# Performance work log

Hardware: AMD Instinct MI355X
Metric: run time of the kernel (lower is better)

## Reference

```python
import jax, jax.numpy as jnp
import numpy as np

W_BIJ, W_ORTH, W_LAP, W_PRE = 1000.0, 1000.0, 1.0, 100000.0
N, V, C, K = 8, 5000, 128, 128
NUM_DESC = int(C * 0.2)  # 25, matches sub_pre=0.2


def setup_inputs() -> dict:
    key = jax.random.key(0)
    ks = jax.random.split(key, 10)
    return {
        "C12": jax.random.normal(ks[0], (N, K, K), jnp.float32) * 0.1,
        "C21": jax.random.normal(ks[1], (N, K, K), jnp.float32) * 0.1,
        "feat_1": jax.random.normal(ks[2], (N, V, C), jnp.float32),
        "feat_2": jax.random.normal(ks[3], (N, V, C), jnp.float32),
        "evecs_1": jax.random.normal(ks[4], (N, V, K), jnp.float32) * 0.02,
        "evecs_2": jax.random.normal(ks[5], (N, V, K), jnp.float32) * 0.02,
        "evecs_trans1": jax.random.normal(ks[6], (N, K, V), jnp.float32) * 0.02,
        "evecs_trans2": jax.random.normal(ks[7], (N, K, V), jnp.float32) * 0.02,
        "evals_1": jax.random.uniform(ks[8], (N, K), jnp.float32),
        "evals_2": jax.random.uniform(ks[9], (N, K), jnp.float32),
        "desc_ind": jnp.arange(NUM_DESC, dtype=jnp.int32),
    }


def _frob3(a, b):
    # torch FrobeniusLoss on [N,K,K]: mean over batch of sum((a-b)^2, dims (1,2))
    return jnp.mean(jnp.sum((a - b) ** 2, axis=(1, 2)))


def reference(C12, C21, feat_1, feat_2, evecs_1, evecs_2,
              evecs_trans1, evecs_trans2, evals_1, evals_2, desc_ind):
    n, k, _ = C12.shape
    eye = jnp.eye(k, dtype=C12.dtype)[None]  # broadcasts over batch

    l_bij = (_frob3(jnp.einsum('nij,njk->nik', C12, C21), eye)
             + _frob3(jnp.einsum('nij,njk->nik', C21, C12), eye)) * W_BIJ

    l_orth = (_frob3(jnp.einsum('nji,njk->nik', C12, C12), eye)
              + _frob3(jnp.einsum('nji,njk->nik', C21, C21), eye)) * W_ORTH

    # diag-scale commutativity: C * evals (col scale) vs evals * C (row scale)
    l_lap = (_frob3(C12 * evals_1[:, None, :], evals_2[:, :, None] * C12)
             + _frob3(C21 * evals_2[:, None, :], evals_1[:, :, None] * C21)) * W_LAP

    # descriptor preservation via commutativity, D = num_desc subsampled channels
    f1 = feat_1[:, :, desc_ind]  # [N,V,D]
    f2 = feat_2[:, :, desc_ind]
    # M[n,d] = Phi_trans @ diag(f[:,d]) @ Phi  (KxK per descriptor), fused einsum
    M1 = jnp.einsum('nkv,nvd,nvj->ndkj', evecs_trans1, f1, evecs_1)
    M2 = jnp.einsum('nkv,nvd,nvj->ndkj', evecs_trans2, f2, evecs_2)
    s1 = jnp.einsum('nij,ndjk->ndik', C12, M1)  # C12 @ M1_d
    t1 = jnp.einsum('ndij,njk->ndik', M2, C12)  # M2_d @ C12
    s2 = jnp.einsum('nij,ndjk->ndik', C21, M2)
    t2 = jnp.einsum('ndij,njk->ndik', M1, C21)
    # torch FrobeniusLoss on 5D [N,D,1,K,K]: sum over axes (1,2), then global mean
    # over remaining [N,K,K] -> total_sum / (N*K*K)
    denom = jnp.asarray(n * k * k, s1.dtype)
    l_pre = ((jnp.sum((s1 - t1) ** 2) + jnp.sum((s2 - t2) ** 2)) / denom) * W_PRE

    return jnp.stack([l_bij, l_orth, l_lap, l_pre])
```

## Files before the change

### kernel.cpp

```cpp
#include <hip/hip_runtime.h>

typedef float v4f __attribute__((ext_vector_type(4)));
typedef unsigned int u32;
typedef __attribute__((ext_vector_type(2))) u32 u32x2;
typedef __attribute__((ext_vector_type(4))) u32 u32x4;
typedef __attribute__((ext_vector_type(8))) short bhalf8;

#define K 128
#define W_BIJ 1000.0f
#define W_ORTH 1000.0f
#define W_LAP 1.0f
#define W_PRE 100000.0f

#define NCH 79
#define TILE_B 16384
#define CTILE_B 32768
#define VPAD 5120

union B8 { u32x4 u; bhalf8 h; };

static __device__ __forceinline__ unsigned short f2b(float x) {
    union { float f; unsigned int u; } v; v.f = x;
    unsigned int u = v.u + 0x7FFFu + ((v.u >> 16) & 1u);
    return (unsigned short)(u >> 16);
}
static __device__ __forceinline__ u32 pk2(float lo, float hi) {
    return (u32)f2b(lo) | ((u32)f2b(hi) << 16);
}
static __device__ __forceinline__ float bitsf(u32 x) {
    union { u32 u; float f; } v; v.u = x; return v.f;
}
static __device__ __forceinline__ u32 cvtpk(float lo, float hi) {
    u32 r; asm("v_cvt_pk_bf16_f32 %0, %1, %2" : "=v"(r) : "v"(lo), "v"(hi)); return r;
}
static __device__ __forceinline__ void gload_lds16(const void* g, void* l) {
    __builtin_amdgcn_global_load_lds((const __attribute__((address_space(1))) u32*)g,
                                     (__attribute__((address_space(3))) u32*)l, 16, 0, 0);
}

extern "C" __global__ __launch_bounds__(256, 2)
void surfm_conv(const float* __restrict__ T1, const float* __restrict__ T2,
                const float* __restrict__ E1, const float* __restrict__ E2,
                const float* __restrict__ F1, const float* __restrict__ F2,
                const float* __restrict__ C12g, const float* __restrict__ C21g,
                const int* __restrict__ desc,
                unsigned short* __restrict__ Abf, unsigned short* __restrict__ Ebf,
                float* __restrict__ Fbf, char* __restrict__ Cbf,
                int V, int CF)
{
    __shared__ char csm[36992];
    const int b = blockIdx.x;
    const int tid = threadIdx.x;

    if (b < 1264) {
        const int c  = b % NCH;
        const int mn = b / NCH;
        const float* src = ((mn & 8) ? T2 : T1) + (size_t)(mn & 7) * K * V;
        char* dst = (char*)Abf + (size_t)b * TILE_B;
        #pragma unroll
        for (int it = 0; it < 4; ++it) {
            const int item = it * 256 + tid;
            const int grp = item & 7, r = item >> 3;
            const int kg = grp ^ (r & 7);
            const int k = c * 64 + kg * 8;
            u32x4 o = (u32x4){0u,0u,0u,0u};
            if (k + 8 <= V) {
                const v4f lo = *(const v4f*)(src + (size_t)r * V + k);
                const v4f hi = *(const v4f*)(src + (size_t)r * V + k + 4);
                o[0] = pk2(lo[0], lo[1]); o[1] = pk2(lo[2], lo[3]);
                o[2] = pk2(hi[0], hi[1]); o[3] = pk2(hi[2], hi[3]);
            }
            *(u32x4*)(dst + r * 128 + grp * 16) = o;
        }
    } else if (b < 2528) {
        const int idx = b - 1264;
        const int c  = idx % NCH;
        const int mn = idx / NCH;
        const float* src = ((mn & 8) ? E2 : E1) + (size_t)(mn & 7) * V * K;
        char* dst = (char*)Ebf + (size_t)idx * TILE_B;
        #pragma unroll
        for (int it = 0; it < 8; ++it) {
            const int item = it * 256 + tid;
            const int vp = item >> 5;
            const int j4 = (item & 31) * 4;
            const int v = c * 64 + vp * 2;
            v4f e0 = {0.f,0.f,0.f,0.f}, e1 = e0;
            if (v < V)     e0 = *(const v4f*)(src + (size_t)v * K + j4);
            if (v + 1 < V) e1 = *(const v4f*)(src + (size_t)(v + 1) * K + j4);
            #pragma unroll
            for (int e = 0; e < 4; ++e) {
                const int j = j4 + e;
                *(u32*)(csm + j * 128 + vp * 4) = pk2(e0[e], e1[e]);
            }
        }
        __syncthreads();
        #pragma unroll
        for (int it = 0; it < 4; ++it) {
            const int item = it * 256 + tid;
            *(u32x4*)(dst + item * 16) = *(const u32x4*)(csm + item * 16);
        }
    } else if (b < 2928) {
        const int idx = b - 2528;
        const int d  = idx % 25;
        const int mn = idx / 25;
        const int col = desc[d];
        const float* src = ((mn & 8) ? F2 : F1) + (size_t)(mn & 7) * V * CF + col;
        float* dst = Fbf + (size_t)idx * VPAD;
        for (int i = tid; i < VPAD; i += 256)
            dst[i] = (i < V) ? src[(size_t)i * CF] : 0.0f;
    } else {
        const int idx = b - 2928;
        const float* src = ((idx & 8) ? C21g : C12g) + (size_t)(idx & 7) * K * K;
        char* outN = Cbf + (size_t)(idx * 2 + 0) * CTILE_B;
        char* outT = Cbf + (size_t)(idx * 2 + 1) * CTILE_B;
        #pragma unroll
        for (int it = 0; it < 8; ++it) {
            const int item = it * 256 + tid;
            const int r = item >> 4, grp = item & 15;
            const int g = grp ^ (r & 7);
            const v4f lo = *(const v4f*)(src + r * K + g * 8);
            const v4f hi = *(const v4f*)(src + r * K + g * 8 + 4);
            u32x4 o;
            o[0] = pk2(lo[0], lo[1]); o[1] = pk2(lo[2], lo[3]);
            o[2] = pk2(hi[0], hi[1]); o[3] = pk2(hi[2], hi[3]);
            *(u32x4*)(outN + r * 256 + grp * 16) = o;
        }
        #pragma unroll
        for (int it = 0; it < 8; ++it) {
            const int item = it * 256 + tid;
            const int rp = item >> 5;
            const int j4 = (item & 31) * 4;
            const v4f r0 = *(const v4f*)(src + (2 * rp) * K + j4);
            const v4f r1 = *(const v4f*)(src + (2 * rp + 1) * K + j4);
            #pragma unroll
            for (int e = 0; e < 4; ++e) {
                const int j = j4 + e;
                *(u32*)(csm + j * 256 + ((rp * 4) ^ ((j & 7) << 4))) = pk2(r0[e], r1[e]);
            }
        }
        __syncthreads();
        #pragma unroll
        for (int it = 0; it < 8; ++it) {
            const int item = it * 256 + tid;
            *(u32x4*)(outT + item * 16) = *(const u32x4*)(csm + item * 16);
        }
    }
}

extern "C" __global__ __launch_bounds__(512, 4)
void surfm_stage1(const char* __restrict__ Abf, const char* __restrict__ Ebf,
                  const float* __restrict__ Fbf, char* __restrict__ MpartB)
{
    extern __shared__ char sm[];
    const int tid = threadIdx.x;
    const int l  = tid & 63;
    const int wq = __builtin_amdgcn_readfirstlane(tid >> 6);
    const int b = blockIdx.x;
    const int n = b & 7;
    const int rest = b >> 3;
    const int mat = rest & 1;
    const int vq  = (rest >> 1) & 3;
    const int dgi = rest >> 3;
    const int d0 = dgi * 2;
    const bool hasD1 = (d0 + 1) < 25;

    const int mn = mat * 8 + n;
    const char* gA = Abf + (size_t)mn * NCH * TILE_B;
    const char* gE = Ebf + (size_t)mn * NCH * TILE_B;
    const char* gW = (const char*)(Fbf + ((size_t)mn * 25 + d0) * VPAD) + vq * 5120;
    const int c0 = vq * 20;
    const int NT = (vq == 3) ? 19 : 20;

    const int lm = l & 15;
    const int lk = (l >> 4) * 8;
    const int j  = wq * 16 + lm;
    const int rkey = (lm & 7) << 4;
    float* wLds = (float*)(sm + 49152);

    v4f acc0[8], acc1[8];
    #pragma unroll
    for (int mf = 0; mf < 8; ++mf) {
        acc0[mf] = (v4f){0.f,0.f,0.f,0.f};
        acc1[mf] = (v4f){0.f,0.f,0.f,0.f};
    }

    const char* gEl = gE + j * 128 + lk * 2;

    for (int i = wq; i < 10; i += 8)
        gload_lds16(gW + (i / 5) * (VPAD * 4) + (i % 5) * 1024 + l * 16,
                    sm + 49152 + (i / 5) * 5120 + (i % 5) * 1024);
    {
        const char* tA = gA + (size_t)c0 * TILE_B;
        gload_lds16(tA + (wq * 2 + 0) * 1024 + l * 16, sm + (wq * 2 + 0) * 1024);
        gload_lds16(tA + (wq * 2 + 1) * 1024 + l * 16, sm + (wq * 2 + 1) * 1024);
    }
    u32x4 eC0 = *(const u32x4*)(gEl + (size_t)c0 * TILE_B);
    u32x4 eC1 = *(const u32x4*)(gEl + (size_t)c0 * TILE_B + 64);
    {
        const char* tA = gA + (size_t)(c0 + 1) * TILE_B;
        gload_lds16(tA + (wq * 2 + 0) * 1024 + l * 16, sm + 16384 + (wq * 2 + 0) * 1024);
        gload_lds16(tA + (wq * 2 + 1) * 1024 + l * 16, sm + 16384 + (wq * 2 + 1) * 1024);
    }
    asm volatile("s_waitcnt vmcnt(2)" ::: "memory");
    __builtin_amdgcn_s_barrier();

    #pragma unroll 1
    for (int t = 0; t < NT; ++t) {
        const int bufC = t % 3;
        u32x4 eN0 = eC0, eN1 = eC1;
        if (t + 1 < NT) {
            const char* tE = gEl + (size_t)(c0 + t + 1) * TILE_B;
            eN0 = *(const u32x4*)(tE);
            eN1 = *(const u32x4*)(tE + 64);
        }
        if (t + 2 < NT) {
            const char* tA = gA + (size_t)(c0 + t + 2) * TILE_B;
            char* dA = sm + ((t + 2) % 3) * 16384;
            gload_lds16(tA + (wq * 2 + 0) * 1024 + l * 16, dA + (wq * 2 + 0) * 1024);
            gload_lds16(tA + (wq * 2 + 1) * 1024 + l * 16, dA + (wq * 2 + 1) * 1024);
        }
        __builtin_amdgcn_sched_barrier(0);

        const char* Ab = sm + bufC * 16384;
        #pragma unroll
        for (int ks = 0; ks < 2; ++ks) {
            const u32x4 e = ks ? eC1 : eC0;
            const float* pw0 = wLds + t * 64 + ks * 32 + lk;
            const float* pw1 = pw0 + 1280;
            const v4f w0a = *(const v4f*)pw0, w0b = *(const v4f*)(pw0 + 4);
            const v4f w1a = *(const v4f*)pw1, w1b = *(const v4f*)(pw1 + 4);
            const float wl0[4] = {w0a[0], w0a[2], w0b[0], w0b[2]};
            const float wh0[4] = {w0a[1], w0a[3], w0b[1], w0b[3]};
            const float wl1[4] = {w1a[0], w1a[2], w1b[0], w1b[2]};
            const float wh1[4] = {w1a[1], w1a[3], w1b[1], w1b[3]};
            B8 p0, p1;
            #pragma unroll
            for (int t4 = 0; t4 < 4; ++t4) {
                const float elo = bitsf(e[t4] << 16);
                const float ehi = bitsf(e[t4] & 0xFFFF0000u);
                p0.u[t4] = cvtpk(elo * wl0[t4], ehi * wh0[t4]);
                if (hasD1) p1.u[t4] = cvtpk(elo * wl1[t4], ehi * wh1[t4]);
            }
            const int kb = ks * 64 + lk * 2;
            __builtin_amdgcn_s_setprio(1);
            #pragma unroll
            for (int mf = 0; mf < 8; ++mf) {
                const int r = mf * 16 + lm;
                B8 a; a.u = *(const u32x4*)(Ab + r * 128 + (kb ^ rkey));
                acc0[mf] = __builtin_amdgcn_mfma_f32_16x16x32_bf16(a.h, p0.h, acc0[mf], 0, 0, 0);
                if (hasD1)
                    acc1[mf] = __builtin_amdgcn_mfma_f32_16x16x32_bf16(a.h, p1.h, acc1[mf], 0, 0, 0);
            }
            __builtin_amdgcn_s_setprio(0);
        }
        eC0 = eN0; eC1 = eN1;

        if (t + 1 < NT) {
            if (t + 2 < NT) asm volatile("s_waitcnt vmcnt(2)" ::: "memory");
            else            asm volatile("s_waitcnt vmcnt(0)" ::: "memory");
            __builtin_amdgcn_s_barrier();
        }
    }

    const int slotM = (n * 25 + d0) * 2 + mat;
    const int rbyte = (l >> 4) * 8;
    {
        char* dst = MpartB + ((size_t)(vq * 400 + slotM)) * 32768 + j * 256 + rbyte;
        #pragma unroll
        for (int mf = 0; mf < 8; ++mf) {
            u32x2 o;
            o[0] = pk2(acc0[mf][0], acc0[mf][1]);
            o[1] = pk2(acc0[mf][2], acc0[mf][3]);
            *(u32x2*)(dst + mf * 32) = o;
        }
    }
    if (hasD1) {
        char* dst = MpartB + ((size_t)(vq * 400 + slotM + 2)) * 32768 + j * 256 + rbyte;
        #pragma unroll
        for (int mf = 0; mf < 8; ++mf) {
            u32x2 o;
            o[0] = pk2(acc1[mf][0], acc1[mf][1]);
            o[1] = pk2(acc1[mf][2], acc1[mf][3]);
            *(u32x2*)(dst + mf * 32) = o;
        }
    }
}

extern "C" __global__ __launch_bounds__(256, 2)
void surfm_mconv(const char* __restrict__ MpartB, char* __restrict__ Mbf)
{
    extern __shared__ char sm[];
    float* sMT = (float*)sm;
    const int s = blockIdx.x;
    const int tid = threadIdx.x;
    const char* p0 = MpartB + (size_t)s * 32768;
    for (int i = tid; i < 2048; i += 256) {
        const int jj = i >> 4, g = i & 15;
        float sum[8] = {0.f,0.f,0.f,0.f,0.f,0.f,0.f,0.f};
        #pragma unroll
        for (int p = 0; p < 4; ++p) {
            const u32x4 v = *(const u32x4*)(p0 + (size_t)p * 400 * 32768 + jj * 256 + g * 16);
            #pragma unroll
            for (int e = 0; e < 4; ++e) {
                sum[2 * e + 0] += bitsf(v[e] << 16);
                sum[2 * e + 1] += bitsf(v[e] & 0xFFFF0000u);
            }
        }
        float* q = sMT + jj * 132 + g * 8;
        #pragma unroll
        for (int e = 0; e < 8; ++e) q[e] = sum[e];
    }
    __syncthreads();
    char* outN = Mbf + (size_t)s * 65536;
    char* outT = outN + 32768;
    #pragma unroll
    for (int it = 0; it < 16; ++it) {
        const int item = it * 256 + tid;
        const int lay = item >> 11;
        const int g2 = item & 2047;
        const int rr = g2 >> 4, grp = g2 & 15;
        const int g = grp ^ (rr & 7);
        u32x4 o;
        if (lay == 0) {
            const float* p = sMT + rr * 132 + g * 8;
            const v4f a = *(const v4f*)p, bq = *(const v4f*)(p + 4);
            o[0] = pk2(a[0], a[1]);   o[1] = pk2(a[2], a[3]);
            o[2] = pk2(bq[0], bq[1]); o[3] = pk2(bq[2], bq[3]);
            *(u32x4*)(outT + rr * 256 + grp * 16) = o;
        } else {
            const float* p = sMT + (g * 8) * 132 + rr;
            o[0] = pk2(p[0],   p[132]); o[1] = pk2(p[264], p[396]);
            o[2] = pk2(p[528], p[660]); o[3] = pk2(p[792], p[924]);
            *(u32x4*)(outN + rr * 256 + grp * 16) = o;
        }
    }
}

extern "C" __global__ __launch_bounds__(256, 1)
void surfm_stage2(const float* __restrict__ C12g, const float* __restrict__ C21g,
                  const float* __restrict__ ev1g, const float* __restrict__ ev2g,
                  const char* __restrict__ Cbf, const char* __restrict__ Mbf,
                  float* __restrict__ out, int N, int ND)
{
    extern __shared__ char sm[];
    const int b = blockIdx.x;
    const int tid = threadIdx.x;
    const int nPre = N * ND;

    if (b < nPre) {
        const int n = b & 7, d = b >> 3;
        const size_t slot = n * 25 + d;
        const int l = tid & 63;
        const int wq = __builtin_amdgcn_readfirstlane(tid >> 6);
        const int lm = l & 15, lk = (l >> 4) * 8;
        const int wm = wq >> 1, wj = wq & 1;
        float rsum = 0.0f;

        #pragma unroll 1
        for (int ph = 0; ph < 2; ++ph) {
            const char* s0 = Cbf + ((size_t)(ph * 8 + n) * 2 + 0) * CTILE_B;
            const char* s1 = Mbf + (slot * 2 + (ph ? 1 : 0)) * 65536 + 32768;
            const char* s2 = Mbf + (slot * 2 + (ph ? 0 : 1)) * 65536;
            const char* s3 = Cbf + ((size_t)(ph * 8 + n) * 2 + 1) * CTILE_B;
            const char* gs = (wq == 0) ? s0 : (wq == 1) ? s1 : (wq == 2) ? s2 : s3;
            char* ld = sm + wq * 32768;
            if (ph) __builtin_amdgcn_s_barrier();
            #pragma unroll
            for (int i = 0; i < 32; ++i)
                gload_lds16(gs + i * 1024 + l * 16, ld + i * 1024);
            asm volatile("s_waitcnt vmcnt(0)" ::: "memory");
            __builtin_amdgcn_s_barrier();
            __builtin_amdgcn_sched_barrier(0);

            v4f as_[4][4], at_[4][4];
            #pragma unroll
            for (int mf = 0; mf < 4; ++mf)
                #pragma unroll
                for (int jf = 0; jf < 4; ++jf) {
                    as_[mf][jf] = (v4f){0.f,0.f,0.f,0.f};
                    at_[mf][jf] = (v4f){0.f,0.f,0.f,0.f};
                }
            #pragma unroll
            for (int ks = 0; ks < 4; ++ks) {
                const int kb = ks * 64 + lk * 2;
                B8 bS[4], bT[4];
                #pragma unroll
                for (int jf = 0; jf < 4; ++jf) {
                    const int jj = wj * 64 + jf * 16 + lm;
                    const int off = jj * 256 + (kb ^ ((jj & 7) << 4));
                    bS[jf].u = *(const u32x4*)(sm + 32768 + off);
                    bT[jf].u = *(const u32x4*)(sm + 98304 + off);
                }
                #pragma unroll
                for (int mf = 0; mf < 4; ++mf) {
                    const int r = wm * 64 + mf * 16 + lm;
                    const int off = r * 256 + (kb ^ ((r & 7) << 4));
                    B8 aS; aS.u = *(const u32x4*)(sm + off);
                    B8 aT; aT.u = *(const u32x4*)(sm + 65536 + off);
                    #pragma unroll
                    for (int jf = 0; jf < 4; ++jf) {
                        as_[mf][jf] = __builtin_amdgcn_mfma_f32_16x16x32_bf16(aS.h, bS[jf].h, as_[mf][jf], 0, 0, 0);
                        at_[mf][jf] = __builtin_amdgcn_mfma_f32_16x16x32_bf16(aT.h, bT[jf].h, at_[mf][jf], 0, 0, 0);
                    }
                }
            }
            #pragma unroll
            for (int mf = 0; mf < 4; ++mf)
                #pragma unroll
                for (int jf = 0; jf < 4; ++jf) {
                    const v4f df = as_[mf][jf] - at_[mf][jf];
                    rsum += df[0]*df[0] + df[1]*df[1] + df[2]*df[2] + df[3]*df[3];
                }
        }
        #pragma unroll
        for (int off = 32; off; off >>= 1) rsum += __shfl_down(rsum, off, 64);
        if (l == 0)
            atomicAdd(out + 3, rsum * (W_PRE / (float)(N * K * K)));
    } else {
        float* lds = (float*)sm;
        const int idx = b - nPre;
        const int n = idx >> 2, p = idx & 3;
        const float* c12 = C12g + (size_t)n * K * K;
        const float* c21 = C21g + (size_t)n * K * K;
        const float* Xg = (p == 1 || p == 3) ? c21 : c12;
        const float* Yg = (p == 0) ? c21 : c12;
        const float* ea = (p == 0) ? ev1g + n * K : ev2g + n * K;
        const float* eb = (p == 0) ? ev2g + n * K : ev1g + n * K;
        float* X = lds;
        float* Y = lds + K * 129;
        const int tx = tid & 15, ty = tid >> 4;
        float lap = 0.0f;
        for (int i = tid; i < K * K / 4; i += 256) {
            const int r = i >> 5, c4 = (i & 31) * 4;
            const v4f x = *(const v4f*)(Xg + r * K + c4);
            X[r * 129 + c4 + 0] = x[0]; X[r * 129 + c4 + 1] = x[1];
            X[r * 129 + c4 + 2] = x[2]; X[r * 129 + c4 + 3] = x[3];
            if (p < 2) {
                const v4f y = *(const v4f*)(Yg + r * K + c4);
                Y[r * 129 + c4 + 0] = y[0]; Y[r * 129 + c4 + 1] = y[1];
                Y[r * 129 + c4 + 2] = y[2]; Y[r * 129 + c4 + 3] = y[3];
                const float ebi = eb[r];
                #pragma unroll
                for (int e = 0; e < 4; ++e) {
                    const float dlt = ea[c4 + e] - ebi;
                    lap += x[e] * x[e] * dlt * dlt;
                }
            }
        }
        __syncthreads();
        const int i0 = ty * 8, k0 = tx * 8;
        float z[8][8];
        #pragma unroll
        for (int i = 0; i < 8; ++i)
            #pragma unroll
            for (int t = 0; t < 8; ++t) z[i][t] = 0.0f;
        for (int jj = 0; jj < K; ++jj) {
            float xi[8], yk[8];
            if (p < 2) {
                #pragma unroll
                for (int i = 0; i < 8; ++i) xi[i] = X[(i0 + i) * 129 + jj];
                #pragma unroll
                for (int t = 0; t < 8; ++t) yk[t] = Y[jj * 129 + k0 + t];
            } else {
                #pragma unroll
                for (int i = 0; i < 8; ++i) xi[i] = X[jj * 129 + i0 + i];
                #pragma unroll
                for (int t = 0; t < 8; ++t) yk[t] = X[jj * 129 + k0 + t];
            }
            #pragma unroll
            for (int i = 0; i < 8; ++i)
                #pragma unroll
                for (int t = 0; t < 8; ++t) z[i][t] += xi[i] * yk[t];
        }
        float sacc = 0.0f;
        #pragma unroll
        for (int i = 0; i < 8; ++i)
            #pragma unroll
            for (int t = 0; t < 8; ++t) {
                const float e = z[i][t] - ((i0 + i) == (k0 + t) ? 1.0f : 0.0f);
                sacc += e * e;
            }
        #pragma unroll
        for (int off = 32; off; off >>= 1) {
            sacc += __shfl_down(sacc, off, 64);
            lap  += __shfl_down(lap, off, 64);
        }
        if ((tid & 63) == 0) {
            if (p < 2) {
                atomicAdd(out + 0, sacc * (W_BIJ / (float)N));
                atomicAdd(out + 2, lap * (W_LAP / (float)N));
            } else {
                atomicAdd(out + 1, sacc * (W_ORTH / (float)N));
            }
        }
    }
}

extern "C" __global__ __launch_bounds__(256, 1)
void surfm_fused(const float* __restrict__ C12g, const float* __restrict__ C21g,
                 const float* __restrict__ F1, const float* __restrict__ F2,
                 const float* __restrict__ E1g, const float* __restrict__ E2g,
                 const float* __restrict__ T1, const float* __restrict__ T2,
                 const float* __restrict__ ev1g, const float* __restrict__ ev2g,
                 const int* __restrict__ desc, float* __restrict__ out,
                 int N, int ND, int V, int CF)
{
    extern __shared__ char smem[];
    const int b   = blockIdx.x;
    const int tid = threadIdx.x;
    const int nPre = N * ND;

    if (b < nPre) {
        const int n = b & 7;
        const int d = b >> 3;
        const int col = desc[d];
        const float* A1g = T1 + (size_t)n * K * V;
        const float* A2g = T2 + (size_t)n * K * V;
        const float* B1g = E1g + (size_t)n * V * K;
        const float* B2g = E2g + (size_t)n * V * K;
        const float* w1g = F1 + (size_t)n * V * CF;
        const float* w2g = F2 + (size_t)n * V * CF;

        char* As1 = smem;
        char* As2 = smem + 32768;
        char* Bt1 = smem + 65536;
        char* Bt2 = smem + 98304;

        const int l  = tid & 63;
        const int w  = tid >> 6;
        const int lm = l & 15;
        const int lk = (l >> 4) * 8;

        v4f acc1[8][2], acc2[8][2];
        #pragma unroll
        for (int mf = 0; mf < 8; ++mf)
            #pragma unroll
            for (int jf = 0; jf < 2; ++jf) {
                acc1[mf][jf] = (v4f){0.f,0.f,0.f,0.f};
                acc2[mf][jf] = (v4f){0.f,0.f,0.f,0.f};
            }

        for (int v0 = 0; v0 < V; v0 += 128) {
            __syncthreads();
            #pragma unroll 4
            for (int it = 0; it < 16; ++it) {
                const int i  = it * 256 + tid;
                const int r  = i >> 5;
                const int c4 = (i & 31) * 4;
                const int vg = v0 + c4;
                v4f a1 = {0.f,0.f,0.f,0.f}, a2 = {0.f,0.f,0.f,0.f};
                if (vg < V) {
                    a1 = *(const v4f*)(A1g + (size_t)r * V + vg);
                    a2 = *(const v4f*)(A2g + (size_t)r * V + vg);
                }
                const int byte = (r * 256 + c4 * 2) ^ ((r & 7) << 4);
                short4 p1, p2;
                p1.x = (short)f2b(a1[0]); p1.y = (short)f2b(a1[1]);
                p1.z = (short)f2b(a1[2]); p1.w = (short)f2b(a1[3]);
                p2.x = (short)f2b(a2[0]); p2.y = (short)f2b(a2[1]);
                p2.z = (short)f2b(a2[2]); p2.w = (short)f2b(a2[3]);
                *(short4*)(As1 + byte) = p1;
                *(short4*)(As2 + byte) = p2;
            }
            #pragma unroll 2
            for (int it = 0; it < 8; ++it) {
                const int i  = it * 256 + tid;
                const int j4 = (i & 31) * 4;
                const int vp = (i >> 5) * 2;
                const int va = v0 + vp, vb = va + 1;
                v4f e1a = {0.f,0.f,0.f,0.f}, e1b = e1a, e2a = e1a, e2b = e1a;
                if (va < V) {
                    const float w1 = w1g[(size_t)va * CF + col];
                    const float w2 = w2g[(size_t)va * CF + col];
                    e1a = *(const v4f*)(B1g + (size_t)va * K + j4) * w1;
                    e2a = *(const v4f*)(B2g + (size_t)va * K + j4) * w2;
                }
                if (vb < V) {
                    const float w1 = w1g[(size_t)vb * CF + col];
                    const float w2 = w2g[(size_t)vb * CF + col];
                    e1b = *(const v4f*)(B1g + (size_t)vb * K + j4) * w1;
                    e2b = *(const v4f*)(B2g + (size_t)vb * K + j4) * w2;
                }
                #pragma unroll
                for (int e = 0; e < 4; ++e) {
                    const int j = j4 + e;
                    const int key = (((j & 7) ^ ((j >> 3) & 7)) << 4);
                    const int byte = (j * 256 + vp * 2) ^ key;
                    *(u32*)(Bt1 + byte) = pk2(e1a[e], e1b[e]);
                    *(u32*)(Bt2 + byte) = pk2(e2a[e], e2b[e]);
                }
            }
            __syncthreads();
            #pragma unroll
            for (int ks = 0; ks < 4; ++ks) {
                const int k0 = ks * 32 + lk;
                bhalf8 bB1[2], bB2[2];
                #pragma unroll
                for (int jf = 0; jf < 2; ++jf) {
                    const int j = w * 32 + jf * 16 + lm;
                    const int key = (((j & 7) ^ ((j >> 3) & 7)) << 4);
                    const int byte = (j * 256 + k0 * 2) ^ key;
                    bB1[jf] = *(const bhalf8*)(Bt1 + byte);
                    bB2[jf] = *(const bhalf8*)(Bt2 + byte);
                }
                #pragma unroll
                for (int mf = 0; mf < 8; ++mf) {
                    const int r = mf * 16 + lm;
                    const int byte = (r * 256 + k0 * 2) ^ ((r & 7) << 4);
                    const bhalf8 a1 = *(const bhalf8*)(As1 + byte);
                    const bhalf8 a2 = *(const bhalf8*)(As2 + byte);
                    acc1[mf][0] = __builtin_amdgcn_mfma_f32_16x16x32_bf16(a1, bB1[0], acc1[mf][0], 0, 0, 0);
                    acc1[mf][1] = __builtin_amdgcn_mfma_f32_16x16x32_bf16(a1, bB1[1], acc1[mf][1], 0, 0, 0);
                    acc2[mf][0] = __builtin_amdgcn_mfma_f32_16x16x32_bf16(a2, bB2[0], acc2[mf][0], 0, 0, 0);
                    acc2[mf][1] = __builtin_amdgcn_mfma_f32_16x16x32_bf16(a2, bB2[1], acc2[mf][1], 0, 0, 0);
                }
            }
        }
        __syncthreads();
        float* M1 = (float*)smem;
        float* M2 = (float*)smem + K * K;
        #pragma unroll
        for (int mf = 0; mf < 8; ++mf)
            #pragma unroll
            for (int jf = 0; jf < 2; ++jf)
                #pragma unroll
                for (int rg = 0; rg < 4; ++rg) {
                    const int row = mf * 16 + ((l >> 4) << 2) + rg;
                    const int cj  = w * 32 + jf * 16 + lm;
                    const int pc  = ((((cj >> 2) ^ ((row >> 3) & 7)) << 2) | (cj & 3));
                    M1[row * K + pc] = acc1[mf][jf][rg];
                    M2[row * K + pc] = acc2[mf][jf][rg];
                }
        __syncthreads();

        const int tx = tid & 15, ty = tid >> 4;
        const int r0 = ty * 8;
        const int ca = tx * 4, cb = 64 + tx * 4;
        const int kcol = ty & 7;
        const float* c12 = C12g + (size_t)n * K * K;
        const float* c21 = C21g + (size_t)n * K * K;
        v4f acc1a[8], acc1b[8], acc2a[8], acc2b[8];
        #pragma unroll
        for (int i = 0; i < 8; ++i) {
            acc1a[i] = (v4f){0,0,0,0}; acc1b[i] = (v4f){0,0,0,0};
            acc2a[i] = (v4f){0,0,0,0}; acc2b[i] = (v4f){0,0,0,0};
        }
        for (int jj = 0; jj < K; ++jj) {
            const int keyj = (jj >> 3) & 7;
            const int ga = (tx ^ keyj) << 2;
            const int gb = ((16 + tx) ^ keyj) << 2;
            const v4f m1ra = *(const v4f*)(M1 + jj * K + ga);
            const v4f m1rb = *(const v4f*)(M1 + jj * K + gb);
            const v4f m2ra = *(const v4f*)(M2 + jj * K + ga);
            const v4f m2rb = *(const v4f*)(M2 + jj * K + gb);
            const v4f c12ra = *(const v4f*)(c12 + jj * K + ca);
            const v4f c12rb = *(const v4f*)(c12 + jj * K + cb);
            const v4f c21ra = *(const v4f*)(c21 + jj * K + ca);
            const v4f c21rb = *(const v4f*)(c21 + jj * K + cb);
            const int jp = (((jj >> 2) ^ kcol) << 2) | (jj & 3);
            #pragma unroll
            for (int i = 0; i < 8; ++i) {
                const int r = r0 + i;
                const float x12 = c12[r * K + jj];
                const float x21 = c21[r * K + jj];
                const float m1c = M1[r * K + jp];
                const float m2c = M2[r * K + jp];
                acc1a[i] += m1ra * x12; acc1a[i] -= c12ra * m2c;
                acc1b[i] += m1rb * x12; acc1b[i] -= c12rb * m2c;
                acc2a[i] += m2ra * x21; acc2a[i] -= c21ra * m1c;
                acc2b[i] += m2rb * x21; acc2b[i] -= c21rb * m1c;
            }
        }
        float s = 0.0f;
        #pragma unroll
        for (int i = 0; i < 8; ++i)
            #pragma unroll
            for (int e = 0; e < 4; ++e) {
                s += acc1a[i][e] * acc1a[i][e] + acc1b[i][e] * acc1b[i][e];
                s += acc2a[i][e] * acc2a[i][e] + acc2b[i][e] * acc2b[i][e];
            }
        #pragma unroll
        for (int off = 32; off; off >>= 1) s += __shfl_down(s, off, 64);
        if ((tid & 63) == 0)
            atomicAdd(out + 3, s * (W_PRE / (float)(N * K * K)));
    } else {
        float* ldsf = (float*)smem;
        const int idx = b - nPre;
        const int n = idx >> 2, p = idx & 3;
        const float* c12 = C12g + (size_t)n * K * K;
        const float* c21 = C21g + (size_t)n * K * K;
        const float* Xg = (p == 1 || p == 3) ? c21 : c12;
        const float* Yg = (p == 0) ? c21 : c12;
        const float* ea = (p == 0) ? ev1g + n * K : ev2g + n * K;
        const float* eb = (p == 0) ? ev2g + n * K : ev1g + n * K;
        float* X = ldsf;
        float* Y = ldsf + K * 129;
        const int tx = tid & 15, ty = tid >> 4;
        float lap = 0.0f;
        for (int i = tid; i < K * K / 4; i += 256) {
            const int r = i >> 5, c4 = (i & 31) * 4;
            const v4f x = *(const v4f*)(Xg + r * K + c4);
            X[r * 129 + c4 + 0] = x[0]; X[r * 129 + c4 + 1] = x[1];
            X[r * 129 + c4 + 2] = x[2]; X[r * 129 + c4 + 3] = x[3];
            if (p < 2) {
                const v4f y = *(const v4f*)(Yg + r * K + c4);
                Y[r * 129 + c4 + 0] = y[0]; Y[r * 129 + c4 + 1] = y[1];
                Y[r * 129 + c4 + 2] = y[2]; Y[r * 129 + c4 + 3] = y[3];
                const float ebi = eb[r];
                #pragma unroll
                for (int e = 0; e < 4; ++e) {
                    const float dlt = ea[c4 + e] - ebi;
                    lap += x[e] * x[e] * dlt * dlt;
                }
            }
        }
        __syncthreads();
        const int i0 = ty * 8, k0 = tx * 8;
        float z[8][8];
        #pragma unroll
        for (int i = 0; i < 8; ++i)
            #pragma unroll
            for (int t = 0; t < 8; ++t) z[i][t] = 0.0f;
        for (int jj = 0; jj < K; ++jj) {
            float xi[8], yk[8];
            if (p < 2) {
                #pragma unroll
                for (int i = 0; i < 8; ++i) xi[i] = X[(i0 + i) * 129 + jj];
                #pragma unroll
                for (int t = 0; t < 8; ++t) yk[t] = Y[jj * 129 + k0 + t];
            } else {
                #pragma unroll
                for (int i = 0; i < 8; ++i) xi[i] = X[jj * 129 + i0 + i];
                #pragma unroll
                for (int t = 0; t < 8; ++t) yk[t] = X[jj * 129 + k0 + t];
            }
            #pragma unroll
            for (int i = 0; i < 8; ++i)
                #pragma unroll
                for (int t = 0; t < 8; ++t) z[i][t] += xi[i] * yk[t];
        }
        float s = 0.0f;
        #pragma unroll
        for (int i = 0; i < 8; ++i)
            #pragma unroll
            for (int t = 0; t < 8; ++t) {
                const float e = z[i][t] - ((i0 + i) == (k0 + t) ? 1.0f : 0.0f);
                s += e * e;
            }
        #pragma unroll
        for (int off = 32; off; off >>= 1) {
            s   += __shfl_down(s, off, 64);
            lap += __shfl_down(lap, off, 64);
        }
        if ((tid & 63) == 0) {
            if (p < 2) {
                atomicAdd(out + 0, s * (W_BIJ / (float)N));
                atomicAdd(out + 2, lap * (W_LAP / (float)N));
            } else {
                atomicAdd(out + 1, s * (W_ORTH / (float)N));
            }
        }
    }
}

extern "C" void kernel_launch(void* const* d_in, const int* in_sizes, int n_in,
                              void* d_out, int out_size, void* d_ws, size_t ws_size,
                              hipStream_t stream) {
    (void)n_in;
    const float* C12 = (const float*)d_in[0];
    const float* C21 = (const float*)d_in[1];
    const float* F1  = (const float*)d_in[2];
    const float* F2  = (const float*)d_in[3];
    const float* E1  = (const float*)d_in[4];
    const float* E2  = (const float*)d_in[5];
    const float* T1  = (const float*)d_in[6];
    const float* T2  = (const float*)d_in[7];
    const float* ev1 = (const float*)d_in[8];
    const float* ev2 = (const float*)d_in[9];
    const int* desc  = (const int*)d_in[10];
    float* out = (float*)d_out;

    const int N  = in_sizes[8] / K;
    const int ND = in_sizes[10];
    const int V  = in_sizes[4] / (N * K);
    const int CF = in_sizes[2] / (N * V);

    hipMemsetAsync(d_out, 0, (size_t)out_size * sizeof(float), stream);

    const size_t ABF = (size_t)16 * NCH * TILE_B;
    const size_t EBF = ABF;
    const size_t FBF = (size_t)400 * VPAD * 4;
    const size_t CBF = (size_t)32 * CTILE_B;
    const size_t MBF = (size_t)400 * 65536;
    const size_t MPB = (size_t)4 * 400 * 32768;
    const size_t base = ABF + EBF + FBF + CBF + MBF;
    const size_t needPart = base + MPB;

    const bool okShape = (N == 8 && ND == 25 && V == 5000 && CF == 128);
    if (!okShape || ws_size < needPart) {
        const size_t shmem = (size_t)(2 * K * 129) * sizeof(float);
        hipFuncSetAttribute((const void*)surfm_fused,
                            hipFuncAttributeMaxDynamicSharedMemorySize, (int)shmem);
        const int blocks = N * ND + 4 * N;
        surfm_fused<<<blocks, 256, shmem, stream>>>(C12, C21, F1, F2, E1, E2, T1, T2,
                                                    ev1, ev2, desc, out, N, ND, V, CF);
        return;
    }

    char* ws = (char*)d_ws;
    unsigned short* Abf = (unsigned short*)ws;
    unsigned short* Ebf = (unsigned short*)(ws + ABF);
    float* Fbf = (float*)(ws + ABF + EBF);
    char* Cbf = ws + ABF + EBF + FBF;
    char* Mbf = ws + ABF + EBF + FBF + CBF;
    char* MpartB = ws + base;

    surfm_conv<<<2944, 256, 0, stream>>>(T1, T2, E1, E2, F1, F2, C12, C21, desc,
                                         Abf, Ebf, Fbf, Cbf, V, CF);

    const size_t shmem1 = 59392;
    hipFuncSetAttribute((const void*)surfm_stage1,
                        hipFuncAttributeMaxDynamicSharedMemorySize, (int)shmem1);
    surfm_stage1<<<832, 512, shmem1, stream>>>((const char*)Abf, (const char*)Ebf,
                                               Fbf, MpartB);

    const size_t shmemM = (size_t)128 * 132 * 4;
    hipFuncSetAttribute((const void*)surfm_mconv,
                        hipFuncAttributeMaxDynamicSharedMemorySize, (int)shmemM);
    surfm_mconv<<<400, 256, shmemM, stream>>>(MpartB, Mbf);

    const size_t shmem2 = 132096;
    hipFuncSetAttribute((const void*)surfm_stage2,
                        hipFuncAttributeMaxDynamicSharedMemorySize, (int)shmem2);
    surfm_stage2<<<N * ND + 4 * N, 256, shmem2, stream>>>(C12, C21, ev1, ev2,
                                                          Cbf, Mbf, out, N, ND);
}
```

Measured before the change: 189.6 us.

## Switch stage1 operands to fp16 with packed multiply and double-buffered LDS

```diff
diff --git a/kernel.cpp b/kernel.cpp
--- a/kernel.cpp
+++ b/kernel.cpp
@@ -5,6 +5,7 @@
 typedef __attribute__((ext_vector_type(2))) u32 u32x2;
 typedef __attribute__((ext_vector_type(4))) u32 u32x4;
 typedef __attribute__((ext_vector_type(8))) short bhalf8;
+typedef _Float16 half8 __attribute__((ext_vector_type(8)));
 
 #define K 128
 #define W_BIJ 1000.0f
@@ -15,9 +16,11 @@
 #define NCH 79
 #define TILE_B 16384
 #define CTILE_B 32768
-#define VPAD 5120
+#define WSLOT_B 12288
+#define WQ_B 3072
 
 union B8 { u32x4 u; bhalf8 h; };
+union H8 { u32x4 u; half8 h; };
 
 static __device__ __forceinline__ unsigned short f2b(float x) {
     union { float f; unsigned int u; } v; v.f = x;
@@ -27,11 +30,14 @@
 static __device__ __forceinline__ u32 pk2(float lo, float hi) {
     return (u32)f2b(lo) | ((u32)f2b(hi) << 16);
 }
+static __device__ __forceinline__ u32 pkh(float lo, float hi) {
+    u32 r; asm("v_cvt_pkrtz_f16_f32 %0, %1, %2" : "=v"(r) : "v"(lo), "v"(hi)); return r;
+}
+static __device__ __forceinline__ u32 pkmul(u32 a, u32 b) {
+    u32 r; asm("v_pk_mul_f16 %0, %1, %2" : "=v"(r) : "v"(a), "v"(b)); return r;
+}
 static __device__ __forceinline__ float bitsf(u32 x) {
     union { u32 u; float f; } v; v.u = x; return v.f;
-}
-static __device__ __forceinline__ u32 cvtpk(float lo, float hi) {
-    u32 r; asm("v_cvt_pk_bf16_f32 %0, %1, %2" : "=v"(r) : "v"(lo), "v"(hi)); return r;
 }
 static __device__ __forceinline__ void gload_lds16(const void* g, void* l) {
     __builtin_amdgcn_global_load_lds((const __attribute__((address_space(1))) u32*)g,
@@ -45,7 +51,7 @@
                 const float* __restrict__ C12g, const float* __restrict__ C21g,
                 const int* __restrict__ desc,
                 unsigned short* __restrict__ Abf, unsigned short* __restrict__ Ebf,
-                float* __restrict__ Fbf, char* __restrict__ Cbf,
+                char* __restrict__ Fbf, char* __restrict__ Cbf,
                 int V, int CF)
 {
     __shared__ char csm[36992];
@@ -67,8 +73,8 @@
             if (k + 8 <= V) {
                 const v4f lo = *(const v4f*)(src + (size_t)r * V + k);
                 const v4f hi = *(const v4f*)(src + (size_t)r * V + k + 4);
-                o[0] = pk2(lo[0], lo[1]); o[1] = pk2(lo[2], lo[3]);
-                o[2] = pk2(hi[0], hi[1]); o[3] = pk2(hi[2], hi[3]);
+                o[0] = pkh(lo[0], lo[1]); o[1] = pkh(lo[2], lo[3]);
+                o[2] = pkh(hi[0], hi[1]); o[3] = pkh(hi[2], hi[3]);
             }
             *(u32x4*)(dst + r * 128 + grp * 16) = o;
         }
@@ -90,7 +96,7 @@
             #pragma unroll
             for (int e = 0; e < 4; ++e) {
                 const int j = j4 + e;
-                *(u32*)(csm + j * 128 + vp * 4) = pk2(e0[e], e1[e]);
+                *(u32*)(csm + j * 128 + vp * 4) = pkh(e0[e], e1[e]);
             }
         }
         __syncthreads();
@@ -105,9 +111,18 @@
         const int mn = idx / 25;
         const int col = desc[d];
         const float* src = ((mn & 8) ? F2 : F1) + (size_t)(mn & 7) * V * CF + col;
-        float* dst = Fbf + (size_t)idx * VPAD;
-        for (int i = tid; i < VPAD; i += 256)
-            dst[i] = (i < V) ? src[(size_t)i * CF] : 0.0f;
+        u32* dst = (u32*)(Fbf + (size_t)idx * WSLOT_B);
+        for (int i = tid; i < 3072; i += 256) {
+            const int q = i / 768, r = i - q * 768;
+            const int v0 = q * 1280 + r * 2;
+            u32 val = 0u;
+            if (r < 640) {
+                const float f0 = (v0 < V)     ? src[(size_t)v0 * CF]       : 0.f;
+                const float f1 = (v0 + 1 < V) ? src[(size_t)(v0 + 1) * CF] : 0.f;
+                val = pkh(f0, f1);
+            }
+            dst[i] = val;
+        }
     } else {
         const int idx = b - 2928;
         const float* src = ((idx & 8) ? C21g : C12g) + (size_t)(idx & 7) * K * K;
@@ -149,7 +164,7 @@
 
 extern "C" __global__ __launch_bounds__(512, 4)
 void surfm_stage1(const char* __restrict__ Abf, const char* __restrict__ Ebf,
-                  const float* __restrict__ Fbf, char* __restrict__ MpartB)
+                  const char* __restrict__ Fbf, char* __restrict__ MpartB)
 {
     extern __shared__ char sm[];
     const int tid = threadIdx.x;
@@ -167,7 +182,7 @@
     const int mn = mat * 8 + n;
     const char* gA = Abf + (size_t)mn * NCH * TILE_B;
     const char* gE = Ebf + (size_t)mn * NCH * TILE_B;
-    const char* gW = (const char*)(Fbf + ((size_t)mn * 25 + d0) * VPAD) + vq * 5120;
+    const char* gW = Fbf + (size_t)(mn * 25 + d0) * WSLOT_B + vq * WQ_B;
     const int c0 = vq * 20;
     const int NT = (vq == 3) ? 19 : 20;
 
@@ -175,7 +190,7 @@
     const int lk = (l >> 4) * 8;
     const int j  = wq * 16 + lm;
     const int rkey = (lm & 7) << 4;
-    float* wLds = (float*)(sm + 49152);
+    const char* wB = sm + 32768;
 
     v4f acc0[8], acc1[8];
     #pragma unroll
@@ -186,9 +201,10 @@
 
     const char* gEl = gE + j * 128 + lk * 2;
 
-    for (int i = wq; i < 10; i += 8)
-        gload_lds16(gW + (i / 5) * (VPAD * 4) + (i % 5) * 1024 + l * 16,
-                    sm + 49152 + (i / 5) * 5120 + (i % 5) * 1024);
+    for (int i = wq; i < 6; i += 8) {
+        const int dd = i / 3, off = (i - dd * 3) * 1024;
+        gload_lds16(gW + dd * WSLOT_B + off + l * 16, sm + 32768 + dd * WQ_B + off);
+    }
     {
         const char* tA = gA + (size_t)c0 * TILE_B;
         gload_lds16(tA + (wq * 2 + 0) * 1024 + l * 16, sm + (wq * 2 + 0) * 1024);
@@ -196,68 +212,53 @@
     }
     u32x4 eC0 = *(const u32x4*)(gEl + (size_t)c0 * TILE_B);
     u32x4 eC1 = *(const u32x4*)(gEl + (size_t)c0 * TILE_B + 64);
-    {
-        const char* tA = gA + (size_t)(c0 + 1) * TILE_B;
-        gload_lds16(tA + (wq * 2 + 0) * 1024 + l * 16, sm + 16384 + (wq * 2 + 0) * 1024);
-        gload_lds16(tA + (wq * 2 + 1) * 1024 + l * 16, sm + 16384 + (wq * 2 + 1) * 1024);
-    }
-    asm volatile("s_waitcnt vmcnt(2)" ::: "memory");
+    asm volatile("s_waitcnt vmcnt(0)" ::: "memory");
     __builtin_amdgcn_s_barrier();
 
     #pragma unroll 1
     for (int t = 0; t < NT; ++t) {
-        const int bufC = t % 3;
+        const int par = t & 1;
         u32x4 eN0 = eC0, eN1 = eC1;
         if (t + 1 < NT) {
+            const char* tA = gA + (size_t)(c0 + t + 1) * TILE_B;
+            char* dA = sm + (par ^ 1) * 16384;
+            gload_lds16(tA + (wq * 2 + 0) * 1024 + l * 16, dA + (wq * 2 + 0) * 1024);
+            gload_lds16(tA + (wq * 2 + 1) * 1024 + l * 16, dA + (wq * 2 + 1) * 1024);
             const char* tE = gEl + (size_t)(c0 + t + 1) * TILE_B;
             eN0 = *(const u32x4*)(tE);
             eN1 = *(const u32x4*)(tE + 64);
         }
-        if (t + 2 < NT) {
-            const char* tA = gA + (size_t)(c0 + t + 2) * TILE_B;
-            char* dA = sm + ((t + 2) % 3) * 16384;
-            gload_lds16(tA + (wq * 2 + 0) * 1024 + l * 16, dA + (wq * 2 + 0) * 1024);
-            gload_lds16(tA + (wq * 2 + 1) * 1024 + l * 16, dA + (wq * 2 + 1) * 1024);
-        }
-        __builtin_amdgcn_sched_barrier(0);
-
-        const char* Ab = sm + bufC * 16384;
+
+        const char* Ab = sm + par * 16384;
         #pragma unroll
         for (int ks = 0; ks < 2; ++ks) {
             const u32x4 e = ks ? eC1 : eC0;
-            const float* pw0 = wLds + t * 64 + ks * 32 + lk;
-            const float* pw1 = pw0 + 1280;
-            const v4f w0a = *(const v4f*)pw0, w0b = *(const v4f*)(pw0 + 4);
-            const v4f w1a = *(const v4f*)pw1, w1b = *(const v4f*)(pw1 + 4);
-            const float wl0[4] = {w0a[0], w0a[2], w0b[0], w0b[2]};
-            const float wh0[4] = {w0a[1], w0a[3], w0b[1], w0b[3]};
-            const float wl1[4] = {w1a[0], w1a[2], w1b[0], w1b[2]};
-            const float wh1[4] = {w1a[1], w1a[3], w1b[1], w1b[3]};
-            B8 p0, p1;
-            #pragma unroll
-            for (int t4 = 0; t4 < 4; ++t4) {
-                const float elo = bitsf(e[t4] << 16);
-                const float ehi = bitsf(e[t4] & 0xFFFF0000u);
-                p0.u[t4] = cvtpk(elo * wl0[t4], ehi * wh0[t4]);
-                if (hasD1) p1.u[t4] = cvtpk(elo * wl1[t4], ehi * wh1[t4]);
+            const int wbyte = t * 128 + ks * 64 + lk * 2;
+            const u32x4 w0 = *(const u32x4*)(wB + wbyte);
+            H8 p0, p1;
+            #pragma unroll
+            for (int q = 0; q < 4; ++q) p0.u[q] = pkmul(e[q], w0[q]);
+            if (hasD1) {
+                const u32x4 w1 = *(const u32x4*)(wB + WQ_B + wbyte);
+                #pragma unroll
+                for (int q = 0; q < 4; ++q) p1.u[q] = pkmul(e[q], w1[q]);
             }
             const int kb = ks * 64 + lk * 2;
             __builtin_amdgcn_s_setprio(1);
             #pragma unroll
             for (int mf = 0; mf < 8; ++mf) {
                 const int r = mf * 16 + lm;
-                B8 a; a.u = *(const u32x4*)(Ab + r * 128 + (kb ^ rkey));
-                acc0[mf] = __builtin_amdgcn_mfma_f32_16x16x32_bf16(a.h, p0.h, acc0[mf], 0, 0, 0);
+                H8 a; a.u = *(const u32x4*)(Ab + r * 128 + (kb ^ rkey));
+                acc0[mf] = __builtin_amdgcn_mfma_f32_16x16x32_f16(a.h, p0.h, acc0[mf], 0, 0, 0);
                 if (hasD1)
-                    acc1[mf] = __builtin_amdgcn_mfma_f32_16x16x32_bf16(a.h, p1.h, acc1[mf], 0, 0, 0);
+                    acc1[mf] = __builtin_amdgcn_mfma_f32_16x16x32_f16(a.h, p1.h, acc1[mf], 0, 0, 0);
             }
             __builtin_amdgcn_s_setprio(0);
         }
         eC0 = eN0; eC1 = eN1;
 
         if (t + 1 < NT) {
-            if (t + 2 < NT) asm volatile("s_waitcnt vmcnt(2)" ::: "memory");
-            else            asm volatile("s_waitcnt vmcnt(0)" ::: "memory");
+            asm volatile("s_waitcnt vmcnt(0)" ::: "memory");
             __builtin_amdgcn_s_barrier();
         }
     }
@@ -789,7 +790,7 @@
 
     const size_t ABF = (size_t)16 * NCH * TILE_B;
     const size_t EBF = ABF;
-    const size_t FBF = (size_t)400 * VPAD * 4;
+    const size_t FBF = (size_t)400 * WSLOT_B;
     const size_t CBF = (size_t)32 * CTILE_B;
     const size_t MBF = (size_t)400 * 65536;
     const size_t MPB = (size_t)4 * 400 * 32768;
@@ -810,7 +811,7 @@
     char* ws = (char*)d_ws;
     unsigned short* Abf = (unsigned short*)ws;
     unsigned short* Ebf = (unsigned short*)(ws + ABF);
-    float* Fbf = (float*)(ws + ABF + EBF);
+    char* Fbf = ws + ABF + EBF;
     char* Cbf = ws + ABF + EBF + FBF;
     char* Mbf = ws + ABF + EBF + FBF + CBF;
     char* MpartB = ws + base;
@@ -818,7 +819,7 @@
     surfm_conv<<<2944, 256, 0, stream>>>(T1, T2, E1, E2, F1, F2, C12, C21, desc,
                                          Abf, Ebf, Fbf, Cbf, V, CF);
 
-    const size_t shmem1 = 59392;
+    const size_t shmem1 = 38912;
     hipFuncSetAttribute((const void*)surfm_stage1,
                         hipFuncAttributeMaxDynamicSharedMemorySize, (int)shmem1);
     surfm_stage1<<<832, 512, shmem1, stream>>>((const char*)Abf, (const char*)Ebf,
```

New measurement: 181.2 us. 1.05x faster.
